# Kernel tuning notes

Measured on AMD Instinct MI355X. Metric: run time of the kernel, lower is better.

## Reference

```python
import jax, jax.numpy as jnp
import numpy as np


def bilinear_resize(x, out_h, out_w):
    # x: [B, C, H, W]; matches torch F.interpolate(mode='bilinear', align_corners=False)
    B, C, H, W = x.shape
    ry = jnp.clip((jnp.arange(out_h, dtype=jnp.float32) + 0.5) * (H / out_h) - 0.5, 0.0, H - 1)
    rx = jnp.clip((jnp.arange(out_w, dtype=jnp.float32) + 0.5) * (W / out_w) - 0.5, 0.0, W - 1)
    y0 = jnp.floor(ry).astype(jnp.int32); y1 = jnp.minimum(y0 + 1, H - 1)
    x0 = jnp.floor(rx).astype(jnp.int32); x1 = jnp.minimum(x0 + 1, W - 1)
    wy = (ry - y0)[:, None]  # [out_h,1]
    wx = (rx - x0)[None, :]  # [1,out_w]
    r0 = x[:, :, y0, :]; r1 = x[:, :, y1, :]
    v00 = r0[:, :, :, x0]; v01 = r0[:, :, :, x1]
    v10 = r1[:, :, :, x0]; v11 = r1[:, :, :, x1]
    return (v00 * (1 - wx) + v01 * wx) * (1 - wy) + (v10 * (1 - wx) + v11 * wx) * wy


def setup_inputs() -> dict:
    key0 = jax.random.key(0)
    ks = jax.random.split(key0, 16)
    B, N, C, H = 2, 300, 256, 8
    hw_lvl = np.array([[64, 64], [32, 32], [16, 16]], dtype=np.int64)
    L = int((hw_lvl[:, 0] * hw_lvl[:, 1]).sum())  # 5376
    p = lambda k, sh: (0.02 * jax.random.normal(k, sh, dtype=jnp.float32))
    return {
        'query': jax.random.normal(ks[0], (B, N, C), dtype=jnp.float32),
        'key': jax.random.normal(ks[1], (B, L, C), dtype=jnp.float32),
        'value': jax.random.normal(ks[2], (B, L, C), dtype=jnp.float32),
        'key_padding_mask': jnp.zeros((B, L), dtype=bool),
        'hw_lvl': hw_lvl,
        'Wq': p(ks[3], (C, C)), 'Wk': p(ks[4], (C, C)), 'Wv': p(ks[5], (C, C)),
        'Wp': p(ks[6], (C, C)), 'bp': jnp.zeros((C,), jnp.float32),
        'W1': p(ks[7], (H, H)), 'b1': jnp.zeros((H,), jnp.float32),
        'W2': p(ks[8], (H, H)), 'b2': jnp.zeros((H,), jnp.float32),
        'W3': p(ks[9], (H, H)), 'b3': jnp.zeros((H,), jnp.float32),
        'Wm': p(ks[10], (3 * H, 1)), 'bm': jnp.zeros((1,), jnp.float32),
    }


def reference(query, key, value, key_padding_mask, hw_lvl,
              Wq, Wk, Wv, Wp, bp, W1, b1, W2, b2, W3, b3, Wm, bm):
    hw = np.asarray(hw_lvl)
    h1, wd1 = int(hw[0, 0]), int(hw[0, 1])
    h2, wd2 = int(hw[1, 0]), int(hw[1, 1])
    h3, wd3 = int(hw[2, 0]), int(hw[2, 1])
    w1 = h1 * wd1
    w2 = w1 + h2 * wd2
    B, N, C = query.shape
    L = key.shape[1]
    H = W1.shape[0]
    scale = (C // H) ** -0.5

    q = (query @ Wq).reshape(B, N, H, C // H)
    k = (key @ Wk).reshape(B, L, H, C // H)
    v = (value @ Wv).reshape(B, L, H, C // H)
    attn = jnp.einsum('bnhd,blhd->bhnl', q, k) * scale  # [B,H,N,L]

    ap = attn.transpose(0, 2, 3, 1)  # [B,N,L,H]
    f1 = jax.nn.relu(ap[:, :, :w1] @ W1 + b1)                      # [B,N,w1,H]
    f2 = jax.nn.relu(ap[:, :, w1:w2] @ W2 + b2)                    # [B,N,h2*wd2,H]
    f3 = jax.nn.relu(ap[:, :, w2:] @ W3 + b3)                      # [B,N,h3*wd3,H]
    f2 = f2.transpose(0, 1, 3, 2).reshape(B * N, H, h2, wd2)
    f3 = f3.transpose(0, 1, 3, 2).reshape(B * N, H, h3, wd3)
    f2 = bilinear_resize(f2, h1, wd1).transpose(0, 2, 3, 1).reshape(B, N, w1, H)
    f3 = bilinear_resize(f3, h1, wd1).transpose(0, 2, 3, 1).reshape(B, N, w1, H)
    new_feats = jnp.concatenate([f1, f2, f3], axis=-1)             # [B,N,w1,3H]
    mask = jax.nn.relu(new_feats @ Wm + bm)                        # [B,N,w1,1]

    aw = jax.nn.softmax(attn, axis=-1)                             # [B,H,N,L]
    x = jnp.einsum('bhnl,blhd->bnhd', aw, v).reshape(B, N, C)
    x = x @ Wp + bp
    return x, mask
```

## Files before the change

kernel.cpp:

```cpp
#include <hip/hip_runtime.h>
#include <hip/hip_bf16.h>

typedef __hip_bfloat16 bf16;
typedef __attribute__((ext_vector_type(8))) short short8v;
typedef __attribute__((ext_vector_type(8))) unsigned short ushort8v;
typedef __attribute__((ext_vector_type(4))) unsigned short ushort4v;
typedef __attribute__((ext_vector_type(4))) float float4v;

__device__ __forceinline__ float bfu2f(unsigned short u) {
    union { unsigned int i; float f; } v; v.i = ((unsigned int)u) << 16; return v.f;
}
__device__ __forceinline__ unsigned short f2bfu_rn(float x) {
    union { float f; unsigned int i; } u; u.f = x;
    unsigned int r = (u.i + 0x7FFFu + ((u.i >> 16) & 1u)) >> 16;
    return (unsigned short)r;
}

__global__ __launch_bounds__(256) void cast_wt(
    const float* __restrict__ Wq, const float* __restrict__ Wk,
    const float* __restrict__ Wv, const float* __restrict__ Wp,
    unsigned short* __restrict__ wt)
{
    __shared__ unsigned short tile[64][72];
    const float* W = (blockIdx.z == 0) ? Wq : (blockIdx.z == 1) ? Wk
                   : (blockIdx.z == 2) ? Wv : Wp;
    unsigned short* WT = wt + (size_t)blockIdx.z * 65536;
    const int t = threadIdx.x;
    const int k0 = blockIdx.x * 64, n0 = blockIdx.y * 64;
    {
        const int r = t >> 2, cseg = (t & 3) * 16;
        const float* src = W + (size_t)(k0 + r) * 256 + n0 + cseg;
        #pragma unroll
        for (int j = 0; j < 16; ++j) tile[r][cseg + j] = f2bfu_rn(src[j]);
    }
    __syncthreads();
    {
        const int ch = t & 63, lq = t >> 6;
        ushort8v o0, o1;
        #pragma unroll
        for (int i = 0; i < 8; ++i) o0[i] = tile[lq * 16 + i][ch];
        #pragma unroll
        for (int i = 0; i < 8; ++i) o1[i] = tile[lq * 16 + 8 + i][ch];
        unsigned short* dst = WT + (size_t)(n0 + ch) * 256 + k0 + lq * 16;
        *(ushort8v*)(dst)     = o0;
        *(ushort8v*)(dst + 8) = o1;
    }
}

__device__ __forceinline__ void proj_core(
    const float* __restrict__ aptr, const unsigned short* __restrict__ Wt,
    int nc0, int m16, int quad, float4v acc[8])
{
    #pragma unroll
    for (int i = 0; i < 8; ++i) acc[i] = (float4v){0.f, 0.f, 0.f, 0.f};
    #pragma unroll
    for (int ks = 0; ks < 8; ++ks) {
        float4 a0 = *(const float4*)(aptr + ks * 32);
        float4 a1 = *(const float4*)(aptr + ks * 32 + 4);
        short8v af;
        af[0] = (short)f2bfu_rn(a0.x); af[1] = (short)f2bfu_rn(a0.y);
        af[2] = (short)f2bfu_rn(a0.z); af[3] = (short)f2bfu_rn(a0.w);
        af[4] = (short)f2bfu_rn(a1.x); af[5] = (short)f2bfu_rn(a1.y);
        af[6] = (short)f2bfu_rn(a1.z); af[7] = (short)f2bfu_rn(a1.w);
        #pragma unroll
        for (int i = 0; i < 8; ++i) {
            short8v bfr = *(const short8v*)(Wt + (size_t)(nc0 + i * 16 + m16) * 256 + ks * 32 + quad * 8);
            acc[i] = __builtin_amdgcn_mfma_f32_16x16x32_bf16(af, bfr, acc[i], 0, 0, 0);
        }
    }
}

__global__ __launch_bounds__(256) void proj_all(
    const float* __restrict__ q, const float* __restrict__ k, const float* __restrict__ v,
    const unsigned short* __restrict__ wt,
    unsigned short* __restrict__ qb, unsigned short* __restrict__ kb,
    unsigned short* __restrict__ vt)
{
    const int t = threadIdx.x;
    const int wave = t >> 6, lane = t & 63;
    const int m16 = lane & 15, quad = lane >> 4;
    const int msub = (wave & 1) * 16;
    const int nc0 = (wave >> 1) * 128;
    const int bx = blockIdx.x;

    float4v acc[8];
    if (bx < 19) {
        const int m0 = bx * 32;
        const int arow = min(m0 + msub + m16, 599);
        proj_core(q + (size_t)arow * 256 + quad * 8, wt, nc0, m16, quad, acc);
        #pragma unroll
        for (int i = 0; i < 8; ++i)
            #pragma unroll
            for (int r = 0; r < 4; ++r) {
                int m = m0 + msub + quad * 4 + r;
                if (m < 600)
                    qb[(size_t)m * 256 + nc0 + i * 16 + m16] = f2bfu_rn(acc[i][r]);
            }
    } else if (bx < 355) {
        const int m0 = (bx - 19) * 32;
        proj_core(k + (size_t)(m0 + msub + m16) * 256 + quad * 8, wt + 65536, nc0, m16, quad, acc);
        #pragma unroll
        for (int i = 0; i < 8; ++i)
            #pragma unroll
            for (int r = 0; r < 4; ++r) {
                int m = m0 + msub + quad * 4 + r;
                kb[(size_t)m * 256 + nc0 + i * 16 + m16] = f2bfu_rn(acc[i][r]);
            }
    } else {
        const int m0 = (bx - 355) * 32;
        proj_core(v + (size_t)(m0 + msub + m16) * 256 + quad * 8, wt + 131072, nc0, m16, quad, acc);
        const int bb = (m0 >= 5376) ? 1 : 0;
        const int lcol = m0 - bb * 5376 + msub + quad * 4;
        #pragma unroll
        for (int i = 0; i < 8; ++i) {
            const int ch = nc0 + i * 16 + m16;
            ushort4v p;
            #pragma unroll
            for (int r = 0; r < 4; ++r) p[r] = f2bfu_rn(acc[i][r]);
            *(ushort4v*)(vt + (size_t)(bb * 256 + ch) * 5376 + lcol) = p;
        }
    }
}

__global__ __launch_bounds__(512) void attn_fused(
    const unsigned short* __restrict__ qb, const unsigned short* __restrict__ kb,
    const unsigned short* __restrict__ vt,
    const float* __restrict__ W1, const float* __restrict__ b1,
    const float* __restrict__ W2, const float* __restrict__ b2,
    const float* __restrict__ W3, const float* __restrict__ b3,
    const float* __restrict__ Wm, const float* __restrict__ bmp,
    float* __restrict__ f1dot, float* __restrict__ gf,
    float* __restrict__ xbp, float* __restrict__ Sp)
{
    const int STR = 134;
    __shared__ unsigned short probs[8][16 * 134];
    __shared__ float wfc[64], bfc[8], wmf[8];
    __shared__ float bmsS;

    const int t = threadIdx.x;
    const int wave = t >> 6, lane = t & 63;
    const int n0 = blockIdx.x * 16;
    const int b  = blockIdx.y;
    const int zz = blockIdx.z;
    const int h = wave;
    const int m16 = lane & 15, quad = lane >> 4;
    const int lc = zz * 128;
    const float scale = 0.17677669529663687f;

    {
        const float* Wsel; const float* bsel; int wmoff;
        if (zz < 32)      { Wsel = W1; bsel = b1; wmoff = 0; }
        else if (zz < 40) { Wsel = W2; bsel = b2; wmoff = 8; }
        else              { Wsel = W3; bsel = b3; wmoff = 16; }
        if (t < 64) wfc[t] = Wsel[t];
        if (t < 8)  { bfc[t] = bsel[t]; wmf[t] = Wm[wmoff + t]; }
        if (t == 0) bmsS = bmp[0];
    }

    const unsigned short* qp = qb + (size_t)(b * 300 + min(n0 + m16, 299)) * 256 + h * 32 + quad * 8;
    const short8v qfrag = *(const short8v*)qp;

    const unsigned short* kbase = kb + (size_t)(b * 5376) * 256 + h * 32 + quad * 8;
    const unsigned short* vt0 = vt + (size_t)(b * 256 + h * 32 + m16) * 5376;
    const unsigned short* vt1 = vt0 + (size_t)16 * 5376;
    unsigned short* pw = &probs[wave][0];

    #pragma unroll
    for (int i = 0; i < 8; ++i) {
        const int lcol = lc + i * 16 + m16;
        short8v kf = *(const short8v*)(kbase + (size_t)lcol * 256);
        float4v c = {0.f, 0.f, 0.f, 0.f};
        c = __builtin_amdgcn_mfma_f32_16x16x32_bf16(kf, qfrag, c, 0, 0, 0);
        ushort4v pk;
        #pragma unroll
        for (int r = 0; r < 4; ++r) pk[r] = f2bfu_rn(c[r] * scale);
        *(ushort4v*)(pw + m16 * STR + i * 16 + quad * 4) = pk;
    }
    __syncthreads();

    {
        const int n = t >> 5, lt = t & 31;
        const int nn = n0 + n;
        if (nn < 300) {
            ushort4v u[8];
            #pragma unroll
            for (int hp = 0; hp < 8; ++hp)
                u[hp] = *(const ushort4v*)(&probs[hp][0] + n * STR + lt * 4);
            float4 o;
            float* op = (float*)&o;
            #pragma unroll
            for (int j = 0; j < 4; ++j) {
                float acc = (zz < 32) ? bmsS : 0.f;
                #pragma unroll
                for (int hh = 0; hh < 8; ++hh) {
                    float s = bfc[hh];
                    #pragma unroll
                    for (int hp = 0; hp < 8; ++hp) s += bfu2f(u[hp][j]) * wfc[hp * 8 + hh];
                    acc += fmaxf(s, 0.f) * wmf[hh];
                }
                op[j] = acc;
            }
            if (zz < 32) {
                *(float4*)(f1dot + (size_t)(b * 300 + nn) * 4096 + lc + lt * 4) = o;
            } else {
                const int cell = lc - 4096 + lt * 4;
                *(float4*)(gf + (size_t)(b * 300 + nn) * 1280 + cell) = o;
            }
        }
    }

    float4v c0 = {0.f, 0.f, 0.f, 0.f};
    float4v c1 = {0.f, 0.f, 0.f, 0.f};
    float sm = 0.f;
    #pragma unroll
    for (int step = 0; step < 4; ++step) {
        const int lloc = step * 32 + quad * 8;
        ushort8v ua = *(const ushort8v*)(pw + m16 * STR + lloc);
        short8v af;
        #pragma unroll
        for (int j = 0; j < 8; ++j) {
            float e = __expf(bfu2f(ua[j]));
            sm += e;
            af[j] = (short)f2bfu_rn(e);
        }
        const int lg = lc + lloc;
        short8v b0 = *(const short8v*)(vt0 + lg);
        short8v b1v = *(const short8v*)(vt1 + lg);
        c0 = __builtin_amdgcn_mfma_f32_16x16x32_bf16(af, b0, c0, 0, 0, 0);
        c1 = __builtin_amdgcn_mfma_f32_16x16x32_bf16(af, b1v, c1, 0, 0, 0);
    }

    {
        float* xplane = xbp + (size_t)zz * 153600;
        #pragma unroll
        for (int r = 0; r < 4; ++r) {
            const int nn = n0 + quad * 4 + r;
            if (nn < 300) {
                float* o = xplane + (size_t)(b * 300 + nn) * 256 + h * 32 + m16;
                o[0]  = c0[r];
                o[16] = c1[r];
            }
        }
        sm += __shfl_xor(sm, 16);
        sm += __shfl_xor(sm, 32);
        if (lane < 16) {
            const int nn = n0 + lane;
            if (nn < 300)
                Sp[(size_t)zz * 4800 + (size_t)(b * 300 + nn) * 8 + h] = sm;
        }
    }
}

__global__ __launch_bounds__(256) void combine_x(
    const float* __restrict__ xbp, const float* __restrict__ Sp, float* __restrict__ xb)
{
    __shared__ float Sinv[8];
    const int m = blockIdx.x;
    const int t = threadIdx.x;
    if (t < 8) {
        float S = 0.f;
        #pragma unroll 6
        for (int z = 0; z < 42; ++z) S += Sp[(size_t)z * 4800 + (size_t)m * 8 + t];
        Sinv[t] = 1.0f / S;
    }
    __syncthreads();
    float acc = 0.f;
    const float* p = xbp + (size_t)m * 256 + t;
    #pragma unroll 6
    for (int z = 0; z < 42; ++z) acc += p[(size_t)z * 153600];
    xb[(size_t)m * 256 + t] = acc * Sinv[t >> 5];
}

__global__ __launch_bounds__(256) void proj_out(
    const float* __restrict__ xb, const unsigned short* __restrict__ Wtp,
    const float* __restrict__ bp, float* __restrict__ out)
{
    const int t = threadIdx.x;
    const int wave = t >> 6, lane = t & 63;
    const int m16 = lane & 15, quad = lane >> 4;
    const int msub = (wave & 1) * 16;
    const int nc0 = (wave >> 1) * 128;
    const int m0 = blockIdx.x * 32;

    const int arow = min(m0 + msub + m16, 599);
    float4v acc[8];
    proj_core(xb + (size_t)arow * 256 + quad * 8, Wtp, nc0, m16, quad, acc);

    #pragma unroll
    for (int i = 0; i < 8; ++i) {
        const float bv = bp[nc0 + i * 16 + m16];
        #pragma unroll
        for (int r = 0; r < 4; ++r) {
            int m = m0 + msub + quad * 4 + r;
            if (m < 600)
                out[(size_t)m * 256 + nc0 + i * 16 + m16] = acc[i][r] + bv;
        }
    }
}

__global__ __launch_bounds__(256) void mask_lite(
    const float* __restrict__ f1dot, const float* __restrict__ gf,
    float* __restrict__ out)
{
    __shared__ float gs[1280];
    const int t  = threadIdx.x;
    const int bn = blockIdx.x;
    const int ph = blockIdx.y;

    {
        const float4* src = (const float4*)(gf + (size_t)bn * 1280);
        ((float4*)gs)[t] = src[t];
        if (t < 64) ((float4*)gs)[256 + t] = src[256 + t];
    }
    __syncthreads();

    const int p0 = ph * 2048 + t * 8;
    float f[8];
    *(float4*)&f[0] = *(const float4*)(f1dot + (size_t)bn * 4096 + p0);
    *(float4*)&f[4] = *(const float4*)(f1dot + (size_t)bn * 4096 + p0 + 4);

    float res[8];
    #pragma unroll
    for (int pp = 0; pp < 8; ++pp) {
        const int p = p0 + pp;
        const int Y = p >> 6, X = p & 63;
        float acc = f[pp];
        {
            float ry = fminf(fmaxf(0.5f * Y - 0.25f, 0.f), 31.f);
            float rx = fminf(fmaxf(0.5f * X - 0.25f, 0.f), 31.f);
            int y0 = (int)ry, x0 = (int)rx;
            int y1 = min(y0 + 1, 31), x1 = min(x0 + 1, 31);
            float wy = ry - (float)y0, wx = rx - (float)x0;
            acc += (gs[y0 * 32 + x0] * (1.f - wx) + gs[y0 * 32 + x1] * wx) * (1.f - wy)
                 + (gs[y1 * 32 + x0] * (1.f - wx) + gs[y1 * 32 + x1] * wx) * wy;
        }
        {
            float ry = fminf(fmaxf(0.25f * Y - 0.375f, 0.f), 15.f);
            float rx = fminf(fmaxf(0.25f * X - 0.375f, 0.f), 15.f);
            int y0 = (int)ry, x0 = (int)rx;
            int y1 = min(y0 + 1, 15), x1 = min(x0 + 1, 15);
            float wy = ry - (float)y0, wx = rx - (float)x0;
            acc += (gs[1024 + y0 * 16 + x0] * (1.f - wx) + gs[1024 + y0 * 16 + x1] * wx) * (1.f - wy)
                 + (gs[1024 + y1 * 16 + x0] * (1.f - wx) + gs[1024 + y1 * 16 + x1] * wx) * wy;
        }
        res[pp] = fmaxf(acc, 0.f);
    }
    float* o = out + 153600 + (size_t)bn * 4096 + p0;
    *(float4*)(o)     = *(float4*)&res[0];
    *(float4*)(o + 4) = *(float4*)&res[4];
}

extern "C" void kernel_launch(void* const* d_in, const int* in_sizes, int n_in,
                              void* d_out, int out_size, void* d_ws, size_t ws_size,
                              hipStream_t stream) {
    const float* query = (const float*)d_in[0];
    const float* key   = (const float*)d_in[1];
    const float* value = (const float*)d_in[2];
    const float* Wq = (const float*)d_in[5];
    const float* Wk = (const float*)d_in[6];
    const float* Wv = (const float*)d_in[7];
    const float* Wp = (const float*)d_in[8];
    const float* bp = (const float*)d_in[9];
    const float* W1 = (const float*)d_in[10];
    const float* b1 = (const float*)d_in[11];
    const float* W2 = (const float*)d_in[12];
    const float* b2 = (const float*)d_in[13];
    const float* W3 = (const float*)d_in[14];
    const float* b3 = (const float*)d_in[15];
    const float* Wm = (const float*)d_in[16];
    const float* bm = (const float*)d_in[17];
    float* out = (float*)d_out;

    char* ws = (char*)d_ws;
    unsigned short* wt = (unsigned short*)(ws);
    bf16*  qb    = (bf16*) (ws + 524288);
    bf16*  kb    = (bf16*) (ws + 831488);
    bf16*  vt    = (bf16*) (ws + 6336512);
    float* f1dot = (float*)(ws + 11841536);
    float* gf    = (float*)(ws + 21671936);
    float* xbp   = (float*)(ws + 24743936);
    float* Sp    = (float*)(ws + 50548736);
    float* xb    = (float*)(ws + 51355136);

    cast_wt<<<dim3(4, 4, 4), 256, 0, stream>>>(Wq, Wk, Wv, Wp, wt);

    proj_all<<<691, 256, 0, stream>>>(query, key, value, wt,
        (unsigned short*)qb, (unsigned short*)kb, (unsigned short*)vt);

    attn_fused<<<dim3(19, 2, 42), 512, 0, stream>>>(
        (const unsigned short*)qb, (const unsigned short*)kb, (const unsigned short*)vt,
        W1, b1, W2, b2, W3, b3, Wm, bm,
        f1dot, gf, xbp, Sp);

    mask_lite<<<dim3(600, 2), 256, 0, stream>>>(f1dot, gf, out);

    combine_x<<<600, 256, 0, stream>>>(xbp, Sp, xb);

    proj_out<<<19, 256, 0, stream>>>(xb, (const unsigned short*)wt + 196608, bp, out);
}
```

Before: 209.6 us.

## Remap attention grid for XCD locality, nontemporal stores, merge mask and combine kernels

```diff
diff --git a/kernel.cpp b/kernel.cpp
--- a/kernel.cpp
+++ b/kernel.cpp
@@ -137,11 +137,16 @@
     __shared__ float wfc[64], bfc[8], wmf[8];
     __shared__ float bmsS;
 
+    const int i0 = blockIdx.x;
+    const int g = (i0 & 7) * 200 + (i0 >> 3);
+    if (g >= 1596) return;
+    const int zz = g / 38;
+    const int rem = g % 38;
+    const int b = rem / 19;
+    const int n0 = (rem % 19) * 16;
+
     const int t = threadIdx.x;
     const int wave = t >> 6, lane = t & 63;
-    const int n0 = blockIdx.x * 16;
-    const int b  = blockIdx.y;
-    const int zz = blockIdx.z;
     const int h = wave;
     const int m16 = lane & 15, quad = lane >> 4;
     const int lc = zz * 128;
@@ -186,8 +191,7 @@
             #pragma unroll
             for (int hp = 0; hp < 8; ++hp)
                 u[hp] = *(const ushort4v*)(&probs[hp][0] + n * STR + lt * 4);
-            float4 o;
-            float* op = (float*)&o;
+            float4v o;
             #pragma unroll
             for (int j = 0; j < 4; ++j) {
                 float acc = (zz < 32) ? bmsS : 0.f;
@@ -198,13 +202,13 @@
                     for (int hp = 0; hp < 8; ++hp) s += bfu2f(u[hp][j]) * wfc[hp * 8 + hh];
                     acc += fmaxf(s, 0.f) * wmf[hh];
                 }
-                op[j] = acc;
+                o[j] = acc;
             }
             if (zz < 32) {
-                *(float4*)(f1dot + (size_t)(b * 300 + nn) * 4096 + lc + lt * 4) = o;
+                __builtin_nontemporal_store(o, (float4v*)(f1dot + (size_t)(b * 300 + nn) * 4096 + lc + lt * 4));
             } else {
                 const int cell = lc - 4096 + lt * 4;
-                *(float4*)(gf + (size_t)(b * 300 + nn) * 1280 + cell) = o;
+                __builtin_nontemporal_store(o, (float4v*)(gf + (size_t)(b * 300 + nn) * 1280 + cell));
             }
         }
     }
@@ -237,8 +241,8 @@
             const int nn = n0 + quad * 4 + r;
             if (nn < 300) {
                 float* o = xplane + (size_t)(b * 300 + nn) * 256 + h * 32 + m16;
-                o[0]  = c0[r];
-                o[16] = c1[r];
+                __builtin_nontemporal_store(c0[r], o);
+                __builtin_nontemporal_store(c1[r], o + 16);
             }
         }
         sm += __shfl_xor(sm, 16);
@@ -246,67 +250,38 @@
         if (lane < 16) {
             const int nn = n0 + lane;
             if (nn < 300)
-                Sp[(size_t)zz * 4800 + (size_t)(b * 300 + nn) * 8 + h] = sm;
-        }
-    }
-}
-
-__global__ __launch_bounds__(256) void combine_x(
-    const float* __restrict__ xbp, const float* __restrict__ Sp, float* __restrict__ xb)
-{
-    __shared__ float Sinv[8];
-    const int m = blockIdx.x;
-    const int t = threadIdx.x;
-    if (t < 8) {
-        float S = 0.f;
-        #pragma unroll 6
-        for (int z = 0; z < 42; ++z) S += Sp[(size_t)z * 4800 + (size_t)m * 8 + t];
-        Sinv[t] = 1.0f / S;
-    }
-    __syncthreads();
-    float acc = 0.f;
-    const float* p = xbp + (size_t)m * 256 + t;
-    #pragma unroll 6
-    for (int z = 0; z < 42; ++z) acc += p[(size_t)z * 153600];
-    xb[(size_t)m * 256 + t] = acc * Sinv[t >> 5];
-}
-
-__global__ __launch_bounds__(256) void proj_out(
-    const float* __restrict__ xb, const unsigned short* __restrict__ Wtp,
-    const float* __restrict__ bp, float* __restrict__ out)
-{
-    const int t = threadIdx.x;
-    const int wave = t >> 6, lane = t & 63;
-    const int m16 = lane & 15, quad = lane >> 4;
-    const int msub = (wave & 1) * 16;
-    const int nc0 = (wave >> 1) * 128;
-    const int m0 = blockIdx.x * 32;
-
-    const int arow = min(m0 + msub + m16, 599);
-    float4v acc[8];
-    proj_core(xb + (size_t)arow * 256 + quad * 8, Wtp, nc0, m16, quad, acc);
-
-    #pragma unroll
-    for (int i = 0; i < 8; ++i) {
-        const float bv = bp[nc0 + i * 16 + m16];
-        #pragma unroll
-        for (int r = 0; r < 4; ++r) {
-            int m = m0 + msub + quad * 4 + r;
-            if (m < 600)
-                out[(size_t)m * 256 + nc0 + i * 16 + m16] = acc[i][r] + bv;
-        }
-    }
-}
-
-__global__ __launch_bounds__(256) void mask_lite(
+                __builtin_nontemporal_store(sm, Sp + (size_t)zz * 4800 + (size_t)(b * 300 + nn) * 8 + h);
+        }
+    }
+}
+
+__global__ __launch_bounds__(256) void mask_combine(
     const float* __restrict__ f1dot, const float* __restrict__ gf,
-    float* __restrict__ out)
-{
-    __shared__ float gs[1280];
+    const float* __restrict__ xbp, const float* __restrict__ Sp,
+    float* __restrict__ xb, float* __restrict__ out)
+{
     const int t  = threadIdx.x;
     const int bn = blockIdx.x;
     const int ph = blockIdx.y;
 
+    if (ph == 2) {
+        __shared__ float Sinv[8];
+        if (t < 8) {
+            float S = 0.f;
+            #pragma unroll 6
+            for (int z = 0; z < 42; ++z) S += Sp[(size_t)z * 4800 + (size_t)bn * 8 + t];
+            Sinv[t] = 1.0f / S;
+        }
+        __syncthreads();
+        float acc = 0.f;
+        const float* p = xbp + (size_t)bn * 256 + t;
+        #pragma unroll 6
+        for (int z = 0; z < 42; ++z) acc += p[(size_t)z * 153600];
+        xb[(size_t)bn * 256 + t] = acc * Sinv[t >> 5];
+        return;
+    }
+
+    __shared__ float gs[1280];
     {
         const float4* src = (const float4*)(gf + (size_t)bn * 1280);
         ((float4*)gs)[t] = src[t];
@@ -348,6 +323,33 @@
     float* o = out + 153600 + (size_t)bn * 4096 + p0;
     *(float4*)(o)     = *(float4*)&res[0];
     *(float4*)(o + 4) = *(float4*)&res[4];
+}
+
+__global__ __launch_bounds__(256) void proj_out(
+    const float* __restrict__ xb, const unsigned short* __restrict__ Wtp,
+    const float* __restrict__ bp, float* __restrict__ out)
+{
+    const int t = threadIdx.x;
+    const int wave = t >> 6, lane = t & 63;
+    const int m16 = lane & 15, quad = lane >> 4;
+    const int msub = (wave & 1) * 16;
+    const int nc0 = (wave >> 1) * 128;
+    const int m0 = blockIdx.x * 32;
+
+    const int arow = min(m0 + msub + m16, 599);
+    float4v acc[8];
+    proj_core(xb + (size_t)arow * 256 + quad * 8, Wtp, nc0, m16, quad, acc);
+
+    #pragma unroll
+    for (int i = 0; i < 8; ++i) {
+        const float bv = bp[nc0 + i * 16 + m16];
+        #pragma unroll
+        for (int r = 0; r < 4; ++r) {
+            int m = m0 + msub + quad * 4 + r;
+            if (m < 600)
+                out[(size_t)m * 256 + nc0 + i * 16 + m16] = acc[i][r] + bv;
+        }
+    }
 }
 
 extern "C" void kernel_launch(void* const* d_in, const int* in_sizes, int n_in,
@@ -387,14 +389,12 @@
     proj_all<<<691, 256, 0, stream>>>(query, key, value, wt,
         (unsigned short*)qb, (unsigned short*)kb, (unsigned short*)vt);
 
-    attn_fused<<<dim3(19, 2, 42), 512, 0, stream>>>(
+    attn_fused<<<1600, 512, 0, stream>>>(
         (const unsigned short*)qb, (const unsigned short*)kb, (const unsigned short*)vt,
         W1, b1, W2, b2, W3, b3, Wm, bm,
         f1dot, gf, xbp, Sp);
 
-    mask_lite<<<dim3(600, 2), 256, 0, stream>>>(f1dot, gf, out);
-
-    combine_x<<<600, 256, 0, stream>>>(xbp, Sp, xb);
+    mask_combine<<<dim3(600, 3), 256, 0, stream>>>(f1dot, gf, xbp, Sp, xb, out);
 
     proj_out<<<19, 256, 0, stream>>>(xb, (const unsigned short*)wt + 196608, bp, out);
 }
```

New measurement: 205.8 us. No clear change (-1.8%).
